# Kernel optimization log

Measured on AMD Instinct MI355X. Metric: run time of the kernel, lower is better.

The kernel has to match this reference:

```python
import jax, jax.numpy as jnp
import numpy as np

N_NODES = 80000
N_EDGES = 1280000
NODE_DIM = 32
EDGE_DIM = 16
HIDDEN = 64
N_HIDDEN_LAYERS = 3  # layer_count - 1
NUM_GRAPHS = 256


def setup_inputs() -> dict:
    key = jax.random.key(0)
    ks = jax.random.split(key, 16)
    s = 0.05
    H = jax.random.normal(ks[0], (N_NODES, NODE_DIM), dtype=jnp.float32)
    Xe = jax.random.normal(ks[1], (N_EDGES, EDGE_DIM), dtype=jnp.float32)
    id_Xe = jax.random.randint(ks[2], (2, N_EDGES), 0, N_NODES, dtype=jnp.int32).astype(jnp.int64)
    batch_idx = jnp.sort(jax.random.randint(ks[3], (N_NODES,), 0, NUM_GRAPHS, dtype=jnp.int32)).astype(jnp.int64)
    # input layer: M: (node+edge)->hidden, U: (hidden+node)->hidden
    Mw0 = jax.random.normal(ks[4], (NODE_DIM + EDGE_DIM, HIDDEN), dtype=jnp.float32) * s
    Mb0 = jnp.zeros((HIDDEN,), dtype=jnp.float32)
    Uw0 = jax.random.normal(ks[5], (HIDDEN + NODE_DIM, HIDDEN), dtype=jnp.float32) * s
    Ub0 = jnp.zeros((HIDDEN,), dtype=jnp.float32)
    # hidden layers: M: (hidden+edge)->hidden, U: (2*hidden)->hidden (stacked)
    Mw_h = jax.random.normal(ks[6], (N_HIDDEN_LAYERS, HIDDEN + EDGE_DIM, HIDDEN), dtype=jnp.float32) * s
    Mb_h = jnp.zeros((N_HIDDEN_LAYERS, HIDDEN), dtype=jnp.float32)
    Uw_h = jax.random.normal(ks[7], (N_HIDDEN_LAYERS, 2 * HIDDEN, HIDDEN), dtype=jnp.float32) * s
    Ub_h = jnp.zeros((N_HIDDEN_LAYERS, HIDDEN), dtype=jnp.float32)
    # final linear head hidden -> 1
    Ww = jax.random.normal(ks[8], (HIDDEN, 1), dtype=jnp.float32) * s
    Wb = jnp.zeros((1,), dtype=jnp.float32)
    return {"H": H, "Xe": Xe, "id_Xe": id_Xe, "batch_idx": batch_idx,
            "Mw0": Mw0, "Mb0": Mb0, "Uw0": Uw0, "Ub0": Ub0,
            "Mw_h": Mw_h, "Mb_h": Mb_h, "Uw_h": Uw_h, "Ub_h": Ub_h,
            "Ww": Ww, "Wb": Wb}


def reference(H, Xe, id_Xe, batch_idx, Mw0, Mb0, Uw0, Ub0, Mw_h, Mb_h, Uw_h, Ub_h, Ww, Wb):
    n = H.shape[0]
    src = id_Xe[0]
    dst = id_Xe[1]

    def gnn_layer(h, Mw, Mb, Uw, Ub):
        # message: gather source node features, concat edge features, MLP M
        m = jax.nn.relu(jnp.concatenate([h[src], Xe], axis=-1) @ Mw + Mb)  # [E, hidden]
        # scatter-sum to target nodes
        agg = jax.ops.segment_sum(m, dst, num_segments=n)  # [N, hidden]
        # update: concat node state with aggregated message, MLP U
        return jax.nn.relu(jnp.concatenate([h, agg], axis=-1) @ Uw + Ub)

    y = gnn_layer(H, Mw0, Mb0, Uw0, Ub0)
    for i in range(Mw_h.shape[0]):
        y = gnn_layer(y, Mw_h[i], Mb_h[i], Uw_h[i], Ub_h[i])

    pooled = jax.ops.segment_sum(y, batch_idx, num_segments=NUM_GRAPHS)  # [G, hidden]
    return pooled @ Ww + Wb  # [G, 1]
```

## Files before the change

kernel.cpp:

```cpp
#include <hip/hip_runtime.h>
#include <hip/hip_fp16.h>

#define HID 64

struct alignas(8)  H4 { __half2 a, b; };
struct alignas(16) H8 { __half2 h[4]; };

typedef _Float16 f16x8 __attribute__((ext_vector_type(8)));
typedef float    f32x4 __attribute__((ext_vector_type(4)));

__global__ __launch_bounds__(256) void deg_count(const int* __restrict__ dst,
                                                 int* __restrict__ deg, int E) {
    int e = blockIdx.x * 256 + threadIdx.x;
    if (e < E) atomicAdd(&deg[dst[e]], 1);
}

__global__ __launch_bounds__(256) void scan1(const int* __restrict__ deg,
                                             int* __restrict__ rowptr,
                                             int* __restrict__ bsums, int N) {
    __shared__ int s[256];
    const int t = threadIdx.x;
    const int base = blockIdx.x * 2048 + t * 8;
    int v[8], tot = 0;
    #pragma unroll
    for (int i = 0; i < 8; i++) {
        int x = (base + i < N) ? deg[base + i] : 0;
        v[i] = tot; tot += x;
    }
    s[t] = tot; __syncthreads();
    for (int off = 1; off < 256; off <<= 1) {
        int a = (t >= off) ? s[t - off] : 0;
        __syncthreads(); s[t] += a; __syncthreads();
    }
    const int texcl = s[t] - tot;
    #pragma unroll
    for (int i = 0; i < 8; i++)
        if (base + i < N) rowptr[base + i] = texcl + v[i];
    if (t == 255) bsums[blockIdx.x] = s[255];
}

__global__ void scan2(int* bsums, int NB) {
    if (blockIdx.x == 0 && threadIdx.x == 0) {
        int run = 0;
        for (int i = 0; i < NB; i++) { int x = bsums[i]; bsums[i] = run; run += x; }
    }
}

__global__ __launch_bounds__(256) void scan3(int* __restrict__ rowptr,
                                             const int* __restrict__ bsums,
                                             int N, int E) {
    int idx = blockIdx.x * 256 + threadIdx.x;
    if (idx < N) rowptr[idx] += bsums[idx >> 11];
    if (idx == 0) rowptr[N] = E;
}

__global__ __launch_bounds__(256) void permute_k(
    const int* __restrict__ src, const int* __restrict__ dst,
    const int* __restrict__ rowptr, int* __restrict__ cursor,
    const float* __restrict__ Xe, __half* __restrict__ Xes,
    unsigned* __restrict__ pks, int E)
{
    int e = blockIdx.x * 256 + threadIdx.x;
    if (e >= E) return;
    int d = dst[e];
    int pos = rowptr[d] + atomicAdd(&cursor[d], 1);
    pks[pos] = ((unsigned)src[e] << 6) | (unsigned)(d & 63);
    const float4* xi = (const float4*)&Xe[(size_t)e * 16];
    float4 x0 = xi[0], x1 = xi[1], x2 = xi[2], x3 = xi[3];
    H8 h0, h1;
    h0.h[0] = __float22half2_rn(make_float2(x0.x, x0.y));
    h0.h[1] = __float22half2_rn(make_float2(x0.z, x0.w));
    h0.h[2] = __float22half2_rn(make_float2(x1.x, x1.y));
    h0.h[3] = __float22half2_rn(make_float2(x1.z, x1.w));
    h1.h[0] = __float22half2_rn(make_float2(x2.x, x2.y));
    h1.h[1] = __float22half2_rn(make_float2(x2.z, x2.w));
    h1.h[2] = __float22half2_rn(make_float2(x3.x, x3.y));
    h1.h[3] = __float22half2_rn(make_float2(x3.z, x3.w));
    H8* xo = (H8*)&Xes[(size_t)pos * 16];
    xo[0] = h0; xo[1] = h1;
}

template<int K1>
__global__ __launch_bounds__(256) void pm_dual(
    const float* __restrict__ Hn,
    const float* __restrict__ Wm, const float* __restrict__ bm,
    const float* __restrict__ Wu, const float* __restrict__ bu,
    __half* __restrict__ PMs, __half* __restrict__ Th, int N)
{
    constexpr int KP = K1 + 4;
    constexpr int P4 = K1 / 4;
    __shared__ float Ws[K1 * 128];
    __shared__ float Xs[32 * KP];

    const int tid = threadIdx.x;
    for (int i = tid; i < K1 * 32; i += 256) {
        const int row = i >> 5, c4 = i & 31;
        float4 v = (c4 < 16) ? *(const float4*)&Wm[row * 64 + c4 * 4]
                             : *(const float4*)&Wu[row * 64 + (c4 - 16) * 4];
        *(float4*)&Ws[row * 128 + c4 * 4] = v;
    }
    const int nbase = blockIdx.x * 32;
    for (int i = tid; i < 32 * P4; i += 256) {
        const int nl = i / P4, part = i % P4;
        const int n = nbase + nl;
        if (n < N)
            *(float4*)&Xs[nl * KP + part * 4] =
                *(const float4*)&Hn[(size_t)n * K1 + part * 4];
    }
    __syncthreads();

    const int c0 = (tid & 31) * 4;
    const int n0 = (tid >> 5) * 4;
    const float4 bv = (c0 < 64) ? *(const float4*)&bm[c0]
                                : *(const float4*)&bu[c0 - 64];

    float4 acc[4];
    #pragma unroll
    for (int i = 0; i < 4; i++) acc[i] = bv;

    #pragma unroll 4
    for (int k = 0; k < K1; k += 4) {
        const float4 w0 = *(const float4*)&Ws[(k + 0) * 128 + c0];
        const float4 w1 = *(const float4*)&Ws[(k + 1) * 128 + c0];
        const float4 w2 = *(const float4*)&Ws[(k + 2) * 128 + c0];
        const float4 w3 = *(const float4*)&Ws[(k + 3) * 128 + c0];
        #pragma unroll
        for (int ni = 0; ni < 4; ni++) {
            const float4 xv = *(const float4*)&Xs[(n0 + ni) * KP + k];
            acc[ni].x += xv.x * w0.x + xv.y * w1.x + xv.z * w2.x + xv.w * w3.x;
            acc[ni].y += xv.x * w0.y + xv.y * w1.y + xv.z * w2.y + xv.w * w3.y;
            acc[ni].z += xv.x * w0.z + xv.y * w1.z + xv.z * w2.z + xv.w * w3.z;
            acc[ni].w += xv.x * w0.w + xv.y * w1.w + xv.z * w2.w + xv.w * w3.w;
        }
    }

    #pragma unroll
    for (int ni = 0; ni < 4; ni++) {
        const int n = nbase + n0 + ni;
        if (n < N) {
            if (c0 < 64) {
                const int cb = c0 & 15, hb = c0 >> 4;
                PMs[(size_t)n * 64 + (cb + 0) * 4 + hb] = __float2half_rn(acc[ni].x);
                PMs[(size_t)n * 64 + (cb + 1) * 4 + hb] = __float2half_rn(acc[ni].y);
                PMs[(size_t)n * 64 + (cb + 2) * 4 + hb] = __float2half_rn(acc[ni].z);
                PMs[(size_t)n * 64 + (cb + 3) * 4 + hb] = __float2half_rn(acc[ni].w);
            } else {
                H4 o;
                o.a = __float22half2_rn(make_float2(acc[ni].x, acc[ni].y));
                o.b = __float22half2_rn(make_float2(acc[ni].z, acc[ni].w));
                *(H4*)&Th[(size_t)n * 64 + c0 - 64] = o;
            }
        }
    }
}

__global__ __launch_bounds__(256) void edge_fused(
    const __half*   __restrict__ PMs,
    const __half*   __restrict__ Th,
    const __half*   __restrict__ Xes,
    const unsigned* __restrict__ pks,
    const int*      __restrict__ rowptr,
    const float*    __restrict__ Mwb,
    const float*    __restrict__ Uwb,
    float*          __restrict__ Yout,
    int N, int Etot)
{
    constexpr int AGP = HID + 4;
    __shared__ float aggs[32 * AGP];

    const int tid  = threadIdx.x;
    const int wv   = tid >> 6;
    const int lane = tid & 63;
    const int q    = lane >> 4;
    const int li   = lane & 15;
    const int sl0  = q * 4;

    f16x8 bfr[4];
    #pragma unroll
    for (int b = 0; b < 4; b++) {
        #pragma unroll
        for (int i = 0; i < 8; i++) {
            float w = (q < 2) ? Mwb[(8 * q + i) * 64 + 16 * b + li] : 0.f;
            bfr[b][i] = (_Float16)w;
        }
    }
    const unsigned amask = (q < 2) ? 0xFFFFFFFFu : 0u;

    for (int i = tid; i < 32 * AGP; i += 256) aggs[i] = 0.f;

    const int nbase  = blockIdx.x * 32;
    const int nend   = (nbase + 32 < N) ? nbase + 32 : N;
    const int estart = rowptr[nbase];
    const int eend   = rowptr[nend];
    __syncthreads();

    const int pc0 = estart + wv * 16;
    const int qXl = q * 64 + li;

    unsigned pkv[2];
    uint4    xq[4];
    H4       ph[4][4];
    unsigned ldp[4];

#define LOAD_PKV(B, CB) do {                                                  \
    int e_ = (CB) + qXl; e_ = e_ < Etot - 1 ? e_ : Etot - 1;                  \
    pkv[B] = pks[e_];                                                         \
} while (0)

#define LOAD_XQ(S, CB) do {                                                   \
    int b_ = (CB); b_ = b_ <= Etot - 16 ? b_ : Etot - 16;                     \
    xq[S] = *(const uint4*)((const char*)Xes + (size_t)(b_ + li) * 32         \
                            + ((q & 1) << 4));                                \
} while (0)

#define GATH(S, PB, D4) do {                                                  \
    unsigned l_ = 0;                                                          \
    _Pragma("unroll")                                                         \
    for (int j = 0; j < 4; j++) {                                             \
        unsigned pk_ = (unsigned)__shfl((int)pkv[PB], (D4) * 16 + sl0 + j);   \
        ph[S][j] = *(const H4*)((const char*)PMs +                            \
                                ((size_t)(pk_ >> 6) << 7) + li * 8);          \
        l_ |= (pk_ & 31u) << (8 * j);                                         \
    }                                                                         \
    ldp[S] = l_;                                                              \
} while (0)

#define COMPUTE(S, PCC) do {                                                  \
    uint4 xa = xq[S];                                                         \
    xa.x &= amask; xa.y &= amask; xa.z &= amask; xa.w &= amask;               \
    f16x8 a; __builtin_memcpy(&a, &xa, 16);                                   \
    f32x4 acc0, acc1, acc2, acc3;                                             \
    _Pragma("unroll")                                                         \
    for (int j = 0; j < 4; j++) {                                             \
        const float2 g0 = __half22float2(ph[S][j].a);                         \
        const float2 g1 = __half22float2(ph[S][j].b);                         \
        acc0[j] = g0.x; acc1[j] = g0.y; acc2[j] = g1.x; acc3[j] = g1.y;       \
    }                                                                         \
    acc0 = __builtin_amdgcn_mfma_f32_16x16x32_f16(a, bfr[0], acc0, 0, 0, 0);  \
    acc1 = __builtin_amdgcn_mfma_f32_16x16x32_f16(a, bfr[1], acc1, 0, 0, 0);  \
    acc2 = __builtin_amdgcn_mfma_f32_16x16x32_f16(a, bfr[2], acc2, 0, 0, 0);  \
    acc3 = __builtin_amdgcn_mfma_f32_16x16x32_f16(a, bfr[3], acc3, 0, 0, 0);  \
    int ld_prev = -1;                                                         \
    f32x4 racc = {0.f, 0.f, 0.f, 0.f};                                        \
    _Pragma("unroll")                                                         \
    for (int j = 0; j < 4; j++) {                                             \
        f32x4 v;                                                              \
        v[0] = fmaxf(acc0[j], 0.f); v[1] = fmaxf(acc1[j], 0.f);               \
        v[2] = fmaxf(acc2[j], 0.f); v[3] = fmaxf(acc3[j], 0.f);               \
        const int ld = ((PCC) + sl0 + j < eend)                               \
                     ? (int)((ldp[S] >> (8 * j)) & 31u) : -1;                 \
        if (ld == ld_prev) {                                                  \
            racc[0] += v[0]; racc[1] += v[1];                                 \
            racc[2] += v[2]; racc[3] += v[3];                                 \
        } else {                                                              \
            if (ld_prev >= 0) {                                               \
                float* a_ = &aggs[ld_prev * AGP + li];                        \
                atomicAdd(a_ +  0, racc[0]); atomicAdd(a_ + 16, racc[1]);     \
                atomicAdd(a_ + 32, racc[2]); atomicAdd(a_ + 48, racc[3]);     \
            }                                                                 \
            racc = v; ld_prev = ld;                                           \
        }                                                                     \
    }                                                                         \
    if (ld_prev >= 0) {                                                       \
        float* a_ = &aggs[ld_prev * AGP + li];                                \
        atomicAdd(a_ +  0, racc[0]); atomicAdd(a_ + 16, racc[1]);             \
        atomicAdd(a_ + 32, racc[2]); atomicAdd(a_ + 48, racc[3]);             \
    }                                                                         \
} while (0)

    if (pc0 < eend) {
        LOAD_PKV(0, pc0);
        LOAD_PKV(1, pc0 + 256);
        LOAD_XQ(0, pc0);       LOAD_XQ(1, pc0 + 64);
        LOAD_XQ(2, pc0 + 128); LOAD_XQ(3, pc0 + 192);
        GATH(0, 0, 0);
        GATH(1, 0, 1);

        int pc = pc0;
        while (true) {
            { GATH(2, 0, 2); COMPUTE(0, pc); LOAD_XQ(0, pc + 256); }
            pc += 64; if (pc >= eend) break;
            { GATH(3, 0, 3); COMPUTE(1, pc); LOAD_XQ(1, pc + 256); }
            pc += 64; if (pc >= eend) break;
            { GATH(0, 1, 0); COMPUTE(2, pc); LOAD_XQ(2, pc + 256);
              LOAD_PKV(0, pc + 384); }
            pc += 64; if (pc >= eend) break;
            { GATH(1, 1, 1); COMPUTE(3, pc); LOAD_XQ(3, pc + 256); }
            pc += 64; if (pc >= eend) break;
            { GATH(2, 1, 2); COMPUTE(0, pc); LOAD_XQ(0, pc + 256); }
            pc += 64; if (pc >= eend) break;
            { GATH(3, 1, 3); COMPUTE(1, pc); LOAD_XQ(1, pc + 256); }
            pc += 64; if (pc >= eend) break;
            { GATH(0, 0, 0); COMPUTE(2, pc); LOAD_XQ(2, pc + 256);
              LOAD_PKV(1, pc + 384); }
            pc += 64; if (pc >= eend) break;
            { GATH(1, 0, 1); COMPUTE(3, pc); LOAD_XQ(3, pc + 256); }
            pc += 64; if (pc >= eend) break;
        }
    }

#undef LOAD_PKV
#undef LOAD_XQ
#undef GATH
#undef COMPUTE

    __syncthreads();

    {
        const int c0t = (tid & 15) * 4;
        const int r0  = tid >> 4;
        const int r1  = r0 + 16;
        const int n0g = nbase + r0, n1g = nbase + r1;
        float4 acc0 = make_float4(0.f, 0.f, 0.f, 0.f);
        float4 acc1 = make_float4(0.f, 0.f, 0.f, 0.f);
        if (n0g < N) {
            H4 th = *(const H4*)&Th[(size_t)n0g * 64 + c0t];
            float2 lo = __half22float2(th.a), hi = __half22float2(th.b);
            acc0 = make_float4(lo.x, lo.y, hi.x, hi.y);
        }
        if (n1g < N) {
            H4 th = *(const H4*)&Th[(size_t)n1g * 64 + c0t];
            float2 lo = __half22float2(th.a), hi = __half22float2(th.b);
            acc1 = make_float4(lo.x, lo.y, hi.x, hi.y);
        }
        #pragma unroll 4
        for (int k = 0; k < 64; k += 4) {
            const float4 w0 = *(const float4*)&Uwb[(k + 0) * 64 + c0t];
            const float4 w1 = *(const float4*)&Uwb[(k + 1) * 64 + c0t];
            const float4 w2 = *(const float4*)&Uwb[(k + 2) * 64 + c0t];
            const float4 w3 = *(const float4*)&Uwb[(k + 3) * 64 + c0t];
            const float4 x0 = *(const float4*)&aggs[r0 * AGP + k];
            const float4 x1 = *(const float4*)&aggs[r1 * AGP + k];
            acc0.x += x0.x * w0.x + x0.y * w1.x + x0.z * w2.x + x0.w * w3.x;
            acc0.y += x0.x * w0.y + x0.y * w1.y + x0.z * w2.y + x0.w * w3.y;
            acc0.z += x0.x * w0.z + x0.y * w1.z + x0.z * w2.z + x0.w * w3.z;
            acc0.w += x0.x * w0.w + x0.y * w1.w + x0.z * w2.w + x0.w * w3.w;
            acc1.x += x1.x * w0.x + x1.y * w1.x + x1.z * w2.x + x1.w * w3.x;
            acc1.y += x1.x * w0.y + x1.y * w1.y + x1.z * w2.y + x1.w * w3.y;
            acc1.z += x1.x * w0.z + x1.y * w1.z + x1.z * w2.z + x1.w * w3.z;
            acc1.w += x1.x * w0.w + x1.y * w1.w + x1.z * w2.w + x1.w * w3.w;
        }
        if (n0g < N) {
            float4 o;
            o.x = fmaxf(acc0.x, 0.f); o.y = fmaxf(acc0.y, 0.f);
            o.z = fmaxf(acc0.z, 0.f); o.w = fmaxf(acc0.w, 0.f);
            *(float4*)&Yout[(size_t)n0g * HID + c0t] = o;
        }
        if (n1g < N) {
            float4 o;
            o.x = fmaxf(acc1.x, 0.f); o.y = fmaxf(acc1.y, 0.f);
            o.z = fmaxf(acc1.z, 0.f); o.w = fmaxf(acc1.w, 0.f);
            *(float4*)&Yout[(size_t)n1g * HID + c0t] = o;
        }
    }
}

__global__ __launch_bounds__(256) void pool_head(
    const float* __restrict__ Y, const int* __restrict__ bidx,
    const float* __restrict__ Ww, const float* __restrict__ Wb,
    float* __restrict__ out, int N)
{
    const int g = blockIdx.x;
    int a = 0, b = N;
    while (a < b) { int m = (a + b) >> 1; if (bidx[m] < g) a = m + 1; else b = m; }
    const int lo = a;
    b = N;
    while (a < b) { int m = (a + b) >> 1; if (bidx[m] < g + 1) a = m + 1; else b = m; }
    const int hi = a;

    const int tid = threadIdx.x;
    const int c4 = tid & 15, nl = tid >> 4;
    float4 s = make_float4(0.f, 0.f, 0.f, 0.f);
    for (int n = lo + nl; n < hi; n += 16) {
        const float4 v = *(const float4*)&Y[(size_t)n * HID + c4 * 4];
        s.x += v.x; s.y += v.y; s.z += v.z; s.w += v.w;
    }
    __shared__ float red[16 * 68];
    *(float4*)&red[nl * 68 + c4 * 4] = s;
    __syncthreads();
    if (tid < 64) {
        float t = 0.f;
        #pragma unroll
        for (int r = 0; r < 16; r++) t += red[r * 68 + tid];
        t *= Ww[tid];
        #pragma unroll
        for (int off = 32; off; off >>= 1) t += __shfl_down(t, off);
        if (tid == 0) out[g] = t + Wb[0];
    }
}

extern "C" void kernel_launch(void* const* d_in, const int* in_sizes, int n_in,
                              void* d_out, int out_size, void* d_ws, size_t ws_size,
                              hipStream_t stream) {
    const float* H    = (const float*)d_in[0];
    const float* Xe   = (const float*)d_in[1];
    const int*   ids  = (const int*)d_in[2];
    const int*   bidx = (const int*)d_in[3];
    const float* Mw0  = (const float*)d_in[4];
    const float* Mb0  = (const float*)d_in[5];
    const float* Uw0  = (const float*)d_in[6];
    const float* Ub0  = (const float*)d_in[7];
    const float* MwH  = (const float*)d_in[8];
    const float* MbH  = (const float*)d_in[9];
    const float* UwH  = (const float*)d_in[10];
    const float* UbH  = (const float*)d_in[11];
    const float* Ww   = (const float*)d_in[12];
    const float* Wb   = (const float*)d_in[13];
    float* out = (float*)d_out;

    const int N = in_sizes[0] / 32;
    const int E = in_sizes[1] / 16;
    const int* src = ids;
    const int* dst = ids + E;

    float*  hbuf = (float*)d_ws;
    __half* PMs  = (__half*)(hbuf + (size_t)N * HID);
    __half* Th   = PMs + (size_t)N * HID;
    __half* Xes  = Th  + (size_t)N * HID;
    unsigned* pks = (unsigned*)(Xes + (size_t)E * 16);
    int* rowptr  = (int*)(pks + E);
    int* deg     = rowptr + (N + 1);
    int* bsums   = deg + N;

    const int NB = (N + 2047) / 2048;
    const int eblocks = (E + 255) / 256;
    const int ntile32 = (N + 31) / 32;

    hipMemsetAsync(deg, 0, (size_t)N * sizeof(int), stream);
    deg_count<<<eblocks, 256, 0, stream>>>(dst, deg, E);
    scan1<<<NB, 256, 0, stream>>>(deg, rowptr, bsums, N);
    scan2<<<1, 64, 0, stream>>>(bsums, NB);
    scan3<<<(N + 255) / 256, 256, 0, stream>>>(rowptr, bsums, N, E);
    hipMemsetAsync(deg, 0, (size_t)N * sizeof(int), stream);
    permute_k<<<eblocks, 256, 0, stream>>>(src, dst, rowptr, deg,
                                           Xe, Xes, pks, E);

    pm_dual<32><<<ntile32, 256, 0, stream>>>(H, Mw0, Mb0, Uw0, Ub0, PMs, Th, N);
    edge_fused<<<ntile32, 256, 0, stream>>>(PMs, Th, Xes, pks, rowptr,
                                            Mw0 + 32 * HID, Uw0 + 32 * HID, hbuf, N, E);

    for (int l = 0; l < 3; l++) {
        const float* Mw = MwH + (size_t)l * 80 * HID;
        const float* Uw = UwH + (size_t)l * 128 * HID;
        pm_dual<64><<<ntile32, 256, 0, stream>>>(hbuf, Mw, MbH + (size_t)l * HID,
                                                 Uw, UbH + (size_t)l * HID, PMs, Th, N);
        edge_fused<<<ntile32, 256, 0, stream>>>(PMs, Th, Xes, pks, rowptr,
                                                Mw + 64 * HID, Uw + 64 * HID, hbuf, N, E);
    }

    pool_head<<<256, 256, 0, stream>>>(hbuf, bidx, Ww, Wb, out, N);
}
```

Baseline: 995.0 us.

## Enlarge edge_fused node tile to 64 and deepen gather prefetch pipeline

Each edge_fused block now handles 64 destination nodes instead of 32, with a larger shared aggregation buffer and 6-bit local destination indices in the packed edge keys. The gather pipeline is one stage deeper (three gathers primed before the loop). Edge-feature loads are predicated so only the lanes that use them read memory, which replaces the post-load masking. Load clamps now use the block's own edge range instead of the global edge count. The update GEMM covers four rows per thread. This halves block count and amortises per-block setup and weight loading, at the cost of more LDS, more registers and possibly lower occupancy. It relies on the permute kernel packing at least 6 low bits of local index.

```diff
diff --git a/kernel.cpp b/kernel.cpp
--- a/kernel.cpp
+++ b/kernel.cpp
@@ -165,8 +165,9 @@
     float*          __restrict__ Yout,
     int N, int Etot)
 {
-    constexpr int AGP = HID + 4;
-    __shared__ float aggs[32 * AGP];
+    constexpr int TILE = 64;
+    constexpr int AGP  = HID + 4;
+    __shared__ float aggs[TILE * AGP];
 
     const int tid  = threadIdx.x;
     const int wv   = tid >> 6;
@@ -184,18 +185,19 @@
             bfr[b][i] = (_Float16)w;
         }
     }
-    const unsigned amask = (q < 2) ? 0xFFFFFFFFu : 0u;
-
-    for (int i = tid; i < 32 * AGP; i += 256) aggs[i] = 0.f;
-
-    const int nbase  = blockIdx.x * 32;
-    const int nend   = (nbase + 32 < N) ? nbase + 32 : N;
+
+    for (int i = tid; i < TILE * AGP; i += 256) aggs[i] = 0.f;
+
+    const int nbase  = blockIdx.x * TILE;
+    const int nend   = (nbase + TILE < N) ? nbase + TILE : N;
     const int estart = rowptr[nbase];
     const int eend   = rowptr[nend];
     __syncthreads();
 
-    const int pc0 = estart + wv * 16;
-    const int qXl = q * 64 + li;
+    const int pc0   = estart + wv * 16;
+    const int qXl   = q * 64 + li;
+    const int ecapK = eend - 1;
+    const int ecapX = (eend - 16 > 0) ? eend - 16 : 0;
 
     unsigned pkv[2];
     uint4    xq[4];
@@ -203,14 +205,17 @@
     unsigned ldp[4];
 
 #define LOAD_PKV(B, CB) do {                                                  \
-    int e_ = (CB) + qXl; e_ = e_ < Etot - 1 ? e_ : Etot - 1;                  \
+    int e_ = (CB) + qXl; e_ = e_ < ecapK ? e_ : ecapK;                        \
     pkv[B] = pks[e_];                                                         \
 } while (0)
 
 #define LOAD_XQ(S, CB) do {                                                   \
-    int b_ = (CB); b_ = b_ <= Etot - 16 ? b_ : Etot - 16;                     \
-    xq[S] = *(const uint4*)((const char*)Xes + (size_t)(b_ + li) * 32         \
-                            + ((q & 1) << 4));                                \
+    int b_ = (CB); b_ = b_ <= ecapX ? b_ : ecapX;                             \
+    uint4 t_ = make_uint4(0u, 0u, 0u, 0u);                                    \
+    if (q < 2)                                                                \
+        t_ = *(const uint4*)((const char*)Xes + (size_t)(b_ + li) * 32        \
+                             + (q << 4));                                     \
+    xq[S] = t_;                                                               \
 } while (0)
 
 #define GATH(S, PB, D4) do {                                                  \
@@ -220,15 +225,13 @@
         unsigned pk_ = (unsigned)__shfl((int)pkv[PB], (D4) * 16 + sl0 + j);   \
         ph[S][j] = *(const H4*)((const char*)PMs +                            \
                                 ((size_t)(pk_ >> 6) << 7) + li * 8);          \
-        l_ |= (pk_ & 31u) << (8 * j);                                         \
+        l_ |= (pk_ & 63u) << (8 * j);                                         \
     }                                                                         \
     ldp[S] = l_;                                                              \
 } while (0)
 
 #define COMPUTE(S, PCC) do {                                                  \
-    uint4 xa = xq[S];                                                         \
-    xa.x &= amask; xa.y &= amask; xa.z &= amask; xa.w &= amask;               \
-    f16x8 a; __builtin_memcpy(&a, &xa, 16);                                   \
+    f16x8 a; __builtin_memcpy(&a, &xq[S], 16);                                \
     f32x4 acc0, acc1, acc2, acc3;                                             \
     _Pragma("unroll")                                                         \
     for (int j = 0; j < 4; j++) {                                             \
@@ -248,7 +251,7 @@
         v[0] = fmaxf(acc0[j], 0.f); v[1] = fmaxf(acc1[j], 0.f);               \
         v[2] = fmaxf(acc2[j], 0.f); v[3] = fmaxf(acc3[j], 0.f);               \
         const int ld = ((PCC) + sl0 + j < eend)                               \
-                     ? (int)((ldp[S] >> (8 * j)) & 31u) : -1;                 \
+                     ? (int)((ldp[S] >> (8 * j)) & 63u) : -1;                 \
         if (ld == ld_prev) {                                                  \
             racc[0] += v[0]; racc[1] += v[1];                                 \
             racc[2] += v[2]; racc[3] += v[3];                                 \
@@ -275,26 +278,27 @@
         LOAD_XQ(2, pc0 + 128); LOAD_XQ(3, pc0 + 192);
         GATH(0, 0, 0);
         GATH(1, 0, 1);
+        GATH(2, 0, 2);
 
         int pc = pc0;
         while (true) {
-            { GATH(2, 0, 2); COMPUTE(0, pc); LOAD_XQ(0, pc + 256); }
-            pc += 64; if (pc >= eend) break;
-            { GATH(3, 0, 3); COMPUTE(1, pc); LOAD_XQ(1, pc + 256); }
-            pc += 64; if (pc >= eend) break;
-            { GATH(0, 1, 0); COMPUTE(2, pc); LOAD_XQ(2, pc + 256);
+            { GATH(3, 0, 3); COMPUTE(0, pc); LOAD_XQ(0, pc + 256); }
+            pc += 64; if (pc >= eend) break;
+            { GATH(0, 1, 0); COMPUTE(1, pc); LOAD_XQ(1, pc + 256); }
+            pc += 64; if (pc >= eend) break;
+            { GATH(1, 1, 1); COMPUTE(2, pc); LOAD_XQ(2, pc + 256);
               LOAD_PKV(0, pc + 384); }
             pc += 64; if (pc >= eend) break;
-            { GATH(1, 1, 1); COMPUTE(3, pc); LOAD_XQ(3, pc + 256); }
-            pc += 64; if (pc >= eend) break;
-            { GATH(2, 1, 2); COMPUTE(0, pc); LOAD_XQ(0, pc + 256); }
-            pc += 64; if (pc >= eend) break;
-            { GATH(3, 1, 3); COMPUTE(1, pc); LOAD_XQ(1, pc + 256); }
-            pc += 64; if (pc >= eend) break;
-            { GATH(0, 0, 0); COMPUTE(2, pc); LOAD_XQ(2, pc + 256);
+            { GATH(2, 1, 2); COMPUTE(3, pc); LOAD_XQ(3, pc + 256); }
+            pc += 64; if (pc >= eend) break;
+            { GATH(3, 1, 3); COMPUTE(0, pc); LOAD_XQ(0, pc + 256); }
+            pc += 64; if (pc >= eend) break;
+            { GATH(0, 0, 0); COMPUTE(1, pc); LOAD_XQ(1, pc + 256); }
+            pc += 64; if (pc >= eend) break;
+            { GATH(1, 0, 1); COMPUTE(2, pc); LOAD_XQ(2, pc + 256);
               LOAD_PKV(1, pc + 384); }
             pc += 64; if (pc >= eend) break;
-            { GATH(1, 0, 1); COMPUTE(3, pc); LOAD_XQ(3, pc + 256); }
+            { GATH(2, 0, 2); COMPUTE(3, pc); LOAD_XQ(3, pc + 256); }
             pc += 64; if (pc >= eend) break;
         }
     }
@@ -309,19 +313,17 @@
     {
         const int c0t = (tid & 15) * 4;
         const int r0  = tid >> 4;
-        const int r1  = r0 + 16;
-        const int n0g = nbase + r0, n1g = nbase + r1;
-        float4 acc0 = make_float4(0.f, 0.f, 0.f, 0.f);
-        float4 acc1 = make_float4(0.f, 0.f, 0.f, 0.f);
-        if (n0g < N) {
-            H4 th = *(const H4*)&Th[(size_t)n0g * 64 + c0t];
-            float2 lo = __half22float2(th.a), hi = __half22float2(th.b);
-            acc0 = make_float4(lo.x, lo.y, hi.x, hi.y);
-        }
-        if (n1g < N) {
-            H4 th = *(const H4*)&Th[(size_t)n1g * 64 + c0t];
-            float2 lo = __half22float2(th.a), hi = __half22float2(th.b);
-            acc1 = make_float4(lo.x, lo.y, hi.x, hi.y);
+        float4 acc[4];
+        #pragma unroll
+        for (int j = 0; j < 4; j++) {
+            const int n = nbase + r0 + 16 * j;
+            if (n < N) {
+                H4 th = *(const H4*)&Th[(size_t)n * 64 + c0t];
+                float2 lo = __half22float2(th.a), hi = __half22float2(th.b);
+                acc[j] = make_float4(lo.x, lo.y, hi.x, hi.y);
+            } else {
+                acc[j] = make_float4(0.f, 0.f, 0.f, 0.f);
+            }
         }
         #pragma unroll 4
         for (int k = 0; k < 64; k += 4) {
@@ -329,28 +331,24 @@
             const float4 w1 = *(const float4*)&Uwb[(k + 1) * 64 + c0t];
             const float4 w2 = *(const float4*)&Uwb[(k + 2) * 64 + c0t];
             const float4 w3 = *(const float4*)&Uwb[(k + 3) * 64 + c0t];
-            const float4 x0 = *(const float4*)&aggs[r0 * AGP + k];
-            const float4 x1 = *(const float4*)&aggs[r1 * AGP + k];
-            acc0.x += x0.x * w0.x + x0.y * w1.x + x0.z * w2.x + x0.w * w3.x;
-            acc0.y += x0.x * w0.y + x0.y * w1.y + x0.z * w2.y + x0.w * w3.y;
-            acc0.z += x0.x * w0.z + x0.y * w1.z + x0.z * w2.z + x0.w * w3.z;
-            acc0.w += x0.x * w0.w + x0.y * w1.w + x0.z * w2.w + x0.w * w3.w;
-            acc1.x += x1.x * w0.x + x1.y * w1.x + x1.z * w2.x + x1.w * w3.x;
-            acc1.y += x1.x * w0.y + x1.y * w1.y + x1.z * w2.y + x1.w * w3.y;
-            acc1.z += x1.x * w0.z + x1.y * w1.z + x1.z * w2.z + x1.w * w3.z;
-            acc1.w += x1.x * w0.w + x1.y * w1.w + x1.z * w2.w + x1.w * w3.w;
-        }
-        if (n0g < N) {
-            float4 o;
-            o.x = fmaxf(acc0.x, 0.f); o.y = fmaxf(acc0.y, 0.f);
-            o.z = fmaxf(acc0.z, 0.f); o.w = fmaxf(acc0.w, 0.f);
-            *(float4*)&Yout[(size_t)n0g * HID + c0t] = o;
-        }
-        if (n1g < N) {
-            float4 o;
-            o.x = fmaxf(acc1.x, 0.f); o.y = fmaxf(acc1.y, 0.f);
-            o.z = fmaxf(acc1.z, 0.f); o.w = fmaxf(acc1.w, 0.f);
-            *(float4*)&Yout[(size_t)n1g * HID + c0t] = o;
+            #pragma unroll
+            for (int j = 0; j < 4; j++) {
+                const float4 x = *(const float4*)&aggs[(r0 + 16 * j) * AGP + k];
+                acc[j].x += x.x * w0.x + x.y * w1.x + x.z * w2.x + x.w * w3.x;
+                acc[j].y += x.x * w0.y + x.y * w1.y + x.z * w2.y + x.w * w3.y;
+                acc[j].z += x.x * w0.z + x.y * w1.z + x.z * w2.z + x.w * w3.z;
+                acc[j].w += x.x * w0.w + x.y * w1.w + x.z * w2.w + x.w * w3.w;
+            }
+        }
+        #pragma unroll
+        for (int j = 0; j < 4; j++) {
+            const int n = nbase + r0 + 16 * j;
+            if (n < N) {
+                float4 o;
+                o.x = fmaxf(acc[j].x, 0.f); o.y = fmaxf(acc[j].y, 0.f);
+                o.z = fmaxf(acc[j].z, 0.f); o.w = fmaxf(acc[j].w, 0.f);
+                *(float4*)&Yout[(size_t)n * HID + c0t] = o;
+            }
         }
     }
 }
@@ -425,6 +423,7 @@
     const int NB = (N + 2047) / 2048;
     const int eblocks = (E + 255) / 256;
     const int ntile32 = (N + 31) / 32;
+    const int ntile64 = (N + 63) / 64;
 
     hipMemsetAsync(deg, 0, (size_t)N * sizeof(int), stream);
     deg_count<<<eblocks, 256, 0, stream>>>(dst, deg, E);
@@ -436,7 +435,7 @@
                                            Xe, Xes, pks, E);
 
     pm_dual<32><<<ntile32, 256, 0, stream>>>(H, Mw0, Mb0, Uw0, Ub0, PMs, Th, N);
-    edge_fused<<<ntile32, 256, 0, stream>>>(PMs, Th, Xes, pks, rowptr,
+    edge_fused<<<ntile64, 256, 0, stream>>>(PMs, Th, Xes, pks, rowptr,
                                             Mw0 + 32 * HID, Uw0 + 32 * HID, hbuf, N, E);
 
     for (int l = 0; l < 3; l++) {
@@ -444,7 +443,7 @@
         const float* Uw = UwH + (size_t)l * 128 * HID;
         pm_dual<64><<<ntile32, 256, 0, stream>>>(hbuf, Mw, MbH + (size_t)l * HID,
                                                  Uw, UbH + (size_t)l * HID, PMs, Th, N);
-        edge_fused<<<ntile32, 256, 0, stream>>>(PMs, Th, Xes, pks, rowptr,
+        edge_fused<<<ntile64, 256, 0, stream>>>(PMs, Th, Xes, pks, rowptr,
                                                 Mw + 64 * HID, Uw + 64 * HID, hbuf, N, E);
     }
 
```

After: 1.115 ms. 12.1% more time.
